# Kernel tuning notes

Hardware: AMD Instinct MI355X
Metric: run time of the kernel (lower is better)

The kernel has to match this reference:

```python
import jax, jax.numpy as jnp
import numpy as np

IN_DIM, LATENT = 512, 256
INTER, COMMAND, MOTOR = 18, 12, 3
STATE = INTER + COMMAND + MOTOR  # 33
B, T = 64, 512


def _make_mask(p, k, fanout=None, fanin=None, rng=None):
    # NCP-style sparse wiring: random fanout per source / fanin per destination.
    m = np.zeros((p, k), dtype=np.float32)
    if fanout is not None:
        for i in range(p):
            m[i, rng.choice(k, size=fanout, replace=False)] = 1.0
    if fanin is not None:
        for j in range(k):
            m[rng.choice(p, size=fanin, replace=False), j] = 1.0
    # WiredCfCCell appends dense (all-ones) recurrent block for the layer's own state
    full = np.concatenate([m, np.ones((k, k), np.float32)], axis=0)  # (p+k, k)
    return jnp.asarray(full.T)  # (k, p+k), matches nn.Linear weight layout


def setup_inputs() -> dict:
    key = jax.random.key(0)
    ks = iter(jax.random.split(key, 64))
    def nrm(shape, scale=0.1):
        return jax.random.normal(next(ks), shape, jnp.float32) * scale
    rng = np.random.default_rng(2222)
    inp = {}
    inp["x"] = jax.random.normal(next(ks), (B, T, IN_DIM), jnp.float32)
    inp["fc1_w"] = nrm((LATENT, IN_DIM), 0.02)
    inp["fc1_b"] = nrm((LATENT,))
    inp["lstm_wi"] = nrm((4 * STATE, LATENT), 0.05)
    inp["lstm_bi"] = nrm((4 * STATE,))
    inp["lstm_wh"] = nrm((4 * STATE, STATE))
    dims = [(LATENT, INTER), (INTER, COMMAND), (COMMAND, MOTOR)]
    for l, (p, k) in enumerate(dims):
        for nm in ("ff1w", "ff2w", "taw", "tbw"):
            inp[nm + str(l)] = nrm((k, p + k))
        for nm in ("ff1b", "ff2b", "tab", "tbb"):
            inp[nm + str(l)] = nrm((k,))
    fan = [dict(fanout=6), dict(fanout=4), dict(fanin=6)]
    for l, (p, k) in enumerate(dims):
        inp["mask" + str(l)] = _make_mask(p, k, rng=rng, **fan[l])
    return inp


def _forward(x, fc1_w, fc1_b, lstm_wi, lstm_bi, lstm_wh, layers, masks):
    # fc1 projection (dropout in module is never applied in forward)
    feats = jnp.einsum('btd,ld->btl', x, fc1_w) + fc1_b  # (B,T,LATENT)

    def step(carry, u):  # u: (B, LATENT)
        h, c = carry  # (B, STATE) each
        # mixed-memory LSTM cell (ncps LSTMCell: forget gate bias +1)
        z = u @ lstm_wi.T + lstm_bi + h @ lstm_wh.T
        ia, ig, fg, og = jnp.split(z, 4, axis=-1)
        c = c * jax.nn.sigmoid(fg + 1.0) + jnp.tanh(ia) * jax.nn.sigmoid(ig)
        h = jnp.tanh(c) * jax.nn.sigmoid(og)
        # WiredCfCCell: inter -> command -> motor, each a masked CfC cell (ts=1)
        hs = jnp.split(h, (INTER, INTER + COMMAND), axis=-1)
        inp_l = u
        new_hs = []
        for (w1, b1, w2, b2, aw, ab, bw, bb), m, hl in zip(layers, masks, hs):
            xc = jnp.concatenate([inp_l, hl], axis=-1)
            f1 = jnp.tanh(xc @ (w1 * m).T + b1)
            f2 = jnp.tanh(xc @ (w2 * m).T + b2)
            ti = jax.nn.sigmoid((xc @ aw.T + ab) + (xc @ bw.T + bb))  # t_a*ts + t_b, ts=1
            hl = f1 * (1.0 - ti) + ti * f2
            new_hs.append(hl)
            inp_l = hl
        return (jnp.concatenate(new_hs, axis=-1), c), new_hs[-1]

    h0 = jnp.zeros((x.shape[0], STATE), x.dtype)
    (_, _), ys = jax.lax.scan(step, (h0, h0), feats.transpose(1, 0, 2))
    return ys.transpose(1, 0, 2)  # (B, T, MOTOR)


def reference(x, fc1_w, fc1_b, lstm_wi, lstm_bi, lstm_wh,
              ff1w0, ff2w0, taw0, tbw0, ff1b0, ff2b0, tab0, tbb0,
              ff1w1, ff2w1, taw1, tbw1, ff1b1, ff2b1, tab1, tbb1,
              ff1w2, ff2w2, taw2, tbw2, ff1b2, ff2b2, tab2, tbb2,
              mask0, mask1, mask2):
    layers = [
        (ff1w0, ff1b0, ff2w0, ff2b0, taw0, tab0, tbw0, tbb0),
        (ff1w1, ff1b1, ff2w1, ff2b1, taw1, tab1, tbw1, tbb1),
        (ff1w2, ff1b2, ff2w2, ff2b2, taw2, tab2, tbw2, tbb2),
    ]
    return _forward(x, fc1_w, fc1_b, lstm_wi, lstm_bi, lstm_wh, layers, (mask0, mask1, mask2))
```

## Files before the change

kernel.cpp:

```cpp
#include <hip/hip_runtime.h>
#include <hip/hip_bf16.h>

#define BT 32768
#define TSTEPS 512
#define NBATCH 64
#define KDIM 512
#define NPAD 192
#define NW 192

#define L2E 1.4426950408889634f
#define T2E 2.8853900817779268f

__device__ __forceinline__ float rl(float v, int lane) {
    return __int_as_float(__builtin_amdgcn_readlane(__float_as_int(v), lane));
}
__device__ __forceinline__ float bperm(int byteidx, float v) {
    return __int_as_float(__builtin_amdgcn_ds_bpermute(byteidx, __float_as_int(v)));
}
__device__ __forceinline__ float actf(float x, float s, float sc, float a, float b) {
    float e = exp2f(fmaf(s, x, sc));
    return fmaf(a, __builtin_amdgcn_rcpf(1.f + e), b);
}

__global__ __launch_bounds__(256) void fold_kernel(
    const float* __restrict__ fc1_w, const float* __restrict__ fc1_b,
    const float* __restrict__ lstm_wi, const float* __restrict__ lstm_bi,
    const float* __restrict__ ff1w0, const float* __restrict__ ff2w0,
    const float* __restrict__ taw0, const float* __restrict__ tbw0,
    const float* __restrict__ ff1b0, const float* __restrict__ ff2b0,
    const float* __restrict__ tab0, const float* __restrict__ tbb0,
    const float* __restrict__ mask0,
    float* __restrict__ Wc, float* __restrict__ bc)
{
    const int o = blockIdx.x;
    const int t = threadIdx.x;
    __shared__ float wrow[256];
    __shared__ float red[256];

    float wl = 0.f, b0 = 0.f;
    if (o < 132) { wl = lstm_wi[o * 256 + t]; b0 = lstm_bi[o]; }
    else if (o < 186) {
        const int e = o - 132, m = e / 18, i = e - m * 18;
        if (m == 0)      { wl = ff1w0[i * 274 + t] * mask0[i * 274 + t]; b0 = ff1b0[i]; }
        else if (m == 1) { wl = ff2w0[i * 274 + t] * mask0[i * 274 + t]; b0 = ff2b0[i]; }
        else             { wl = taw0[i * 274 + t] + tbw0[i * 274 + t];   b0 = tab0[i] + tbb0[i]; }
    }
    wrow[t] = wl;
    __syncthreads();

    float acc0 = 0.f, acc1 = 0.f;
    for (int l = 0; l < 256; l++) {
        float w = wrow[l];
        acc0 = fmaf(fc1_w[l * 512 + t], w, acc0);
        acc1 = fmaf(fc1_w[l * 512 + t + 256], w, acc1);
    }
    Wc[(size_t)t * NW + o] = acc0;
    Wc[(size_t)(t + 256) * NW + o] = acc1;

    red[t] = fc1_b[t] * wl;
    __syncthreads();
    for (int s = 128; s > 0; s >>= 1) {
        if (t < s) red[t] += red[t + s];
        __syncthreads();
    }
    if (t == 0) bc[o] = red[0] + b0;
}

__global__ __launch_bounds__(256) void gemm_kernel(
    const float* __restrict__ X, const float* __restrict__ Wc,
    const float* __restrict__ bc, float* __restrict__ P)
{
    __shared__ float As[16][68];
    __shared__ float Bs[16][64];
    const int tid = threadIdx.x;
    const int m0 = blockIdx.x * 64;
    const int n0 = blockIdx.y * 64;
    const int lr = tid >> 2;
    const int lc = (tid & 3) << 2;
    const int wr = tid >> 4;
    const int wc = (tid & 15) << 2;
    const int tm = (tid >> 4) << 2;
    const int tn = (tid & 15) << 2;

    float acc[4][4];
#pragma unroll
    for (int i = 0; i < 4; i++)
#pragma unroll
        for (int j = 0; j < 4; j++) acc[i][j] = 0.f;

    for (int k0 = 0; k0 < KDIM; k0 += 16) {
        float4 av = *(const float4*)(X + (size_t)(m0 + lr) * KDIM + k0 + lc);
        float4 bv = *(const float4*)(Wc + (size_t)(k0 + wr) * NW + n0 + wc);
        __syncthreads();
        As[lc + 0][lr] = av.x; As[lc + 1][lr] = av.y;
        As[lc + 2][lr] = av.z; As[lc + 3][lr] = av.w;
        *(float4*)&Bs[wr][wc] = bv;
        __syncthreads();
#pragma unroll
        for (int k = 0; k < 16; k++) {
            float4 a = *(const float4*)&As[k][tm];
            float4 b = *(const float4*)&Bs[k][tn];
            acc[0][0] = fmaf(a.x, b.x, acc[0][0]); acc[0][1] = fmaf(a.x, b.y, acc[0][1]);
            acc[0][2] = fmaf(a.x, b.z, acc[0][2]); acc[0][3] = fmaf(a.x, b.w, acc[0][3]);
            acc[1][0] = fmaf(a.y, b.x, acc[1][0]); acc[1][1] = fmaf(a.y, b.y, acc[1][1]);
            acc[1][2] = fmaf(a.y, b.z, acc[1][2]); acc[1][3] = fmaf(a.y, b.w, acc[1][3]);
            acc[2][0] = fmaf(a.z, b.x, acc[2][0]); acc[2][1] = fmaf(a.z, b.y, acc[2][1]);
            acc[2][2] = fmaf(a.z, b.z, acc[2][2]); acc[2][3] = fmaf(a.z, b.w, acc[2][3]);
            acc[3][0] = fmaf(a.w, b.x, acc[3][0]); acc[3][1] = fmaf(a.w, b.y, acc[3][1]);
            acc[3][2] = fmaf(a.w, b.z, acc[3][2]); acc[3][3] = fmaf(a.w, b.w, acc[3][3]);
        }
    }

    {
        float4 bias = *(const float4*)(bc + n0 + tn);
#pragma unroll
        for (int i = 0; i < 4; i++) {
            float4 r;
            r.x = acc[i][0] + bias.x; r.y = acc[i][1] + bias.y;
            r.z = acc[i][2] + bias.z; r.w = acc[i][3] + bias.w;
            *(float4*)(P + (size_t)(m0 + tm + i) * NPAD + n0 + tn) = r;
        }
    }
}

__global__ __launch_bounds__(64)
__attribute__((amdgpu_waves_per_eu(1, 1)))
void scan_kernel(
    const float* __restrict__ P, const float* __restrict__ lstm_wh,
    const float* __restrict__ ff1w0, const float* __restrict__ ff2w0,
    const float* __restrict__ taw0, const float* __restrict__ tbw0,
    const float* __restrict__ ff1w1, const float* __restrict__ ff2w1,
    const float* __restrict__ taw1, const float* __restrict__ tbw1,
    const float* __restrict__ ff1b1, const float* __restrict__ ff2b1,
    const float* __restrict__ tab1, const float* __restrict__ tbb1,
    const float* __restrict__ ff1w2, const float* __restrict__ ff2w2,
    const float* __restrict__ taw2, const float* __restrict__ tbw2,
    const float* __restrict__ ff1b2, const float* __restrict__ ff2b2,
    const float* __restrict__ tab2, const float* __restrict__ tbb2,
    const float* __restrict__ mask1, const float* __restrict__ mask2,
    float* __restrict__ out)
{
    const int L = threadIdx.x;
    const int b = blockIdx.x;

    __shared__ float wCt[33 * 4];
    if (L < 33) {
        for (int j = 0; j < 4; j++) wCt[L * 4 + j] = lstm_wh[(128 + j) * 33 + L];
    }
    __syncthreads();
    const int jC = L & 3;

    float wA[33], wB[33];
#pragma unroll
    for (int k = 0; k < 33; k++) {
        wA[k] = lstm_wh[L * 33 + k];
        wB[k] = lstm_wh[(64 + L) * 33 + k];
    }
    float w0[18];
    {
        int e = L - 4; e = (e < 0) ? 0 : ((e > 53) ? 53 : e);
        const int m = e / 18, i = e - m * 18;
        const float* pa = (m == 0) ? ff1w0 : (m == 1) ? ff2w0 : taw0;
#pragma unroll
        for (int k = 0; k < 18; k++) {
            float w = pa[i * 274 + 256 + k];
            if (m == 2) w += tbw0[i * 274 + 256 + k];
            w0[k] = w;
        }
    }
    float w1[30], bias1;
    {
        const int d = (L < 36) ? L : 35;
        const int m = d / 12, i = d - m * 12;
        const float* pa = (m == 0) ? ff1w1 : (m == 1) ? ff2w1 : taw1;
#pragma unroll
        for (int k = 0; k < 30; k++) {
            float w = pa[i * 30 + k];
            if (m == 2) w += tbw1[i * 30 + k];
            else w *= mask1[i * 30 + k];
            w1[k] = w;
        }
        bias1 = (m == 0) ? ff1b1[i] : (m == 1) ? ff2b1[i] : (tab1[i] + tbb1[i]);
    }
    float w2[15], bias2;
    {
        const int d = (L < 9) ? L : 8;
        const int m = d / 3, i = d - m * 3;
        const float* pa = (m == 0) ? ff1w2 : (m == 1) ? ff2w2 : taw2;
#pragma unroll
        for (int k = 0; k < 15; k++) {
            float w = pa[i * 15 + k];
            if (m == 2) w += tbw2[i * 15 + k];
            else w *= mask2[i * 15 + k];
            w2[k] = w;
        }
        bias2 = (m == 0) ? ff1b2[i] : (m == 1) ? ff2b2[i] : (tab2[i] + tbb2[i]);
    }

    const float sA  = (L < 33) ? -T2E : -L2E;
    const float aA  = (L < 33) ? 2.f : 1.f;
    const float bA  = (L < 33) ? -1.f : 0.f;
    const float scB = (L >= 2 && L <= 34) ? -L2E : 0.f;
    const float s0  = (L < 40) ? -T2E : -L2E;
    const float a0c = (L < 40) ? 2.f : 1.f;
    const float b0c = (L < 40) ? -1.f : 0.f;
    const float s1  = (L < 24) ? -T2E : -L2E;
    const float a1c = (L < 24) ? 2.f : 1.f;
    const float b1c = (L < 24) ? -1.f : 0.f;
    const float s2  = (L < 6) ? -T2E : -L2E;
    const float a2c = (L < 6) ? 2.f : 1.f;
    const float b2c = (L < 6) ? -1.f : 0.f;

    const int xIgA = (4 * (33 + L)) & 255;
    const int xIgB = (4 * (L - 31)) & 255;
    const int xFg  = (4 * (2 + L)) & 255;
    const int xOgA = (4 * (35 + L)) & 255;
    const int xOgC = (4 * (L - 29)) & 255;
    const int x0f1 = (4 * (4 + L)) & 255;
    const int x0f2 = (4 * (22 + L)) & 255;
    const int x0ti = (4 * (40 + L)) & 255;
    const int x1f1 = (4 * L) & 255;
    const int x1f2 = (4 * (12 + L)) & 255;
    const int x1ti = (4 * (24 + L)) & 255;
    const int x2f1 = (4 * L) & 255;
    const int x2f2 = (4 * (3 + L)) & 255;
    const int x2ti = (4 * (6 + L)) & 255;

    float h[33];
#pragma unroll
    for (int k = 0; k < 33; k++) h[k] = 0.f;
    float cc = 0.f;

    const float* Pb = P + (size_t)b * TSTEPS * NPAD;
    float c1 = Pb[L], c2 = Pb[64 + L], c3 = Pb[128 + L];
    const float* P1 = Pb + NPAD;
    float n1 = P1[L], n2 = P1[64 + L], n3 = P1[128 + L];
    float* outp = out + (size_t)b * TSTEPS * 3 + L;

#pragma unroll 1
    for (int t = 0; t < TSTEPS; t++) {
        const int tf = (t + 2 < TSTEPS) ? t + 2 : TSTEPS - 1;
        const float* Pf = Pb + (size_t)tf * NPAD;
        const float f1p = Pf[L], f2p = Pf[64 + L], f3p = Pf[128 + L];

        float aA0 = c1, aA1 = 0.f, aB0 = c2, aB1 = 0.f, aC0 = c3, aC1 = 0.f;
#pragma unroll
        for (int k = 0; k < 32; k += 2) {
            aA0 = fmaf(wA[k],     h[k],     aA0);
            aA1 = fmaf(wA[k + 1], h[k + 1], aA1);
            aB0 = fmaf(wB[k],     h[k],     aB0);
            aB1 = fmaf(wB[k + 1], h[k + 1], aB1);
            aC0 = fmaf(wCt[k * 4 + jC],       h[k],     aC0);
            aC1 = fmaf(wCt[(k + 1) * 4 + jC], h[k + 1], aC1);
        }
        aA0 = fmaf(wA[32], h[32], aA0);
        aB0 = fmaf(wB[32], h[32], aB0);
        aC0 = fmaf(wCt[32 * 4 + jC], h[32], aC0);
        const float actA = actf(aA0 + aA1, sA, 0.f, aA, bA);
        const float actB = actf(aB0 + aB1, -L2E, scB, 1.f, 0.f);
        const float actC = actf(aC0 + aC1, -L2E, 0.f, 1.f, 0.f);
        const float gIgA = bperm(xIgA, actA);
        const float gIgB = bperm(xIgB, actB);
        const float gFg  = bperm(xFg, actB);
        const float gOgA = bperm(xOgA, actB);
        const float gOgC = bperm(xOgC, actC);
        const float IG = (L < 31) ? gIgA : gIgB;
        const float OG = (L < 29) ? gOgA : gOgC;
        cc = fmaf(cc, gFg, actA * IG);
        const float hv = actf(cc, -T2E, 0.f, 2.f, -1.f) * OG;

#pragma unroll
        for (int k = 0; k < 33; k++) h[k] = rl(hv, k);

        float l00 = c3, l01 = 0.f;
#pragma unroll
        for (int k = 0; k < 18; k += 2) {
            l00 = fmaf(w0[k],     h[k],     l00);
            l01 = fmaf(w0[k + 1], h[k + 1], l01);
        }
        {
            const float av = actf(l00 + l01, s0, 0.f, a0c, b0c);
            const float f1 = bperm(x0f1, av);
            const float f2 = bperm(x0f2, av);
            const float ti = bperm(x0ti, av);
            const float h0 = fmaf(ti, f2 - f1, f1);
#pragma unroll
            for (int k = 0; k < 18; k++) h[k] = rl(h0, k);
        }

        float l10 = bias1, l11 = 0.f;
#pragma unroll
        for (int k = 0; k < 30; k += 2) {
            l10 = fmaf(w1[k],     h[k],     l10);
            l11 = fmaf(w1[k + 1], h[k + 1], l11);
        }
        {
            const float av = actf(l10 + l11, s1, 0.f, a1c, b1c);
            const float f1 = bperm(x1f1, av);
            const float f2 = bperm(x1f2, av);
            const float ti = bperm(x1ti, av);
            const float h1 = fmaf(ti, f2 - f1, f1);
#pragma unroll
            for (int k = 0; k < 12; k++) h[18 + k] = rl(h1, k);
        }

        float l20 = bias2, l21 = 0.f;
#pragma unroll
        for (int k = 0; k < 14; k += 2) {
            l20 = fmaf(w2[k],     h[18 + k],     l20);
            l21 = fmaf(w2[k + 1], h[18 + k + 1], l21);
        }
        l20 = fmaf(w2[14], h[32], l20);
        {
            const float av = actf(l20 + l21, s2, 0.f, a2c, b2c);
            const float f1 = bperm(x2f1, av);
            const float f2 = bperm(x2f2, av);
            const float ti = bperm(x2ti, av);
            const float h2 = fmaf(ti, f2 - f1, f1);
            if (L < 3) outp[(size_t)t * 3] = h2;
            h[30] = rl(h2, 0); h[31] = rl(h2, 1); h[32] = rl(h2, 2);
        }

        c1 = n1; c2 = n2; c3 = n3;
        n1 = f1p; n2 = f2p; n3 = f3p;
    }
}

extern "C" void kernel_launch(void* const* d_in, const int* in_sizes, int n_in,
                              void* d_out, int out_size, void* d_ws, size_t ws_size,
                              hipStream_t stream) {
    const float* x       = (const float*)d_in[0];
    const float* fc1_w   = (const float*)d_in[1];
    const float* fc1_b   = (const float*)d_in[2];
    const float* lstm_wi = (const float*)d_in[3];
    const float* lstm_bi = (const float*)d_in[4];
    const float* lstm_wh = (const float*)d_in[5];
    const float* ff1w0 = (const float*)d_in[6];
    const float* ff2w0 = (const float*)d_in[7];
    const float* taw0  = (const float*)d_in[8];
    const float* tbw0  = (const float*)d_in[9];
    const float* ff1b0 = (const float*)d_in[10];
    const float* ff2b0 = (const float*)d_in[11];
    const float* tab0  = (const float*)d_in[12];
    const float* tbb0  = (const float*)d_in[13];
    const float* ff1w1 = (const float*)d_in[14];
    const float* ff2w1 = (const float*)d_in[15];
    const float* taw1  = (const float*)d_in[16];
    const float* tbw1  = (const float*)d_in[17];
    const float* ff1b1 = (const float*)d_in[18];
    const float* ff2b1 = (const float*)d_in[19];
    const float* tab1  = (const float*)d_in[20];
    const float* tbb1  = (const float*)d_in[21];
    const float* ff1w2 = (const float*)d_in[22];
    const float* ff2w2 = (const float*)d_in[23];
    const float* taw2  = (const float*)d_in[24];
    const float* tbw2  = (const float*)d_in[25];
    const float* ff1b2 = (const float*)d_in[26];
    const float* ff2b2 = (const float*)d_in[27];
    const float* tab2  = (const float*)d_in[28];
    const float* tbb2  = (const float*)d_in[29];
    const float* mask0 = (const float*)d_in[30];
    const float* mask1 = (const float*)d_in[31];
    const float* mask2 = (const float*)d_in[32];

    float* Wc = (float*)d_ws;
    float* bc = Wc + 512 * NW;
    float* P  = bc + NW;
    float* outp = (float*)d_out;

    fold_kernel<<<192, 256, 0, stream>>>(fc1_w, fc1_b, lstm_wi, lstm_bi,
                                         ff1w0, ff2w0, taw0, tbw0,
                                         ff1b0, ff2b0, tab0, tbb0, mask0, Wc, bc);
    gemm_kernel<<<dim3(BT / 64, 3), 256, 0, stream>>>(x, Wc, bc, P);
    scan_kernel<<<NBATCH, 64, 0, stream>>>(P, lstm_wh,
                                           ff1w0, ff2w0, taw0, tbw0,
                                           ff1w1, ff2w1, taw1, tbw1,
                                           ff1b1, ff2b1, tab1, tbb1,
                                           ff1w2, ff2w2, taw2, tbw2,
                                           ff1b2, ff2b2, tab2, tbb2,
                                           mask1, mask2, outp);
}
```

Before: 685.3 us.

## Interleave next-step LSTM gate accumulation into layer chain and split dot-product accumulators

Moves the LSTM recurrent gate dot products for the next timestep so they are accumulated piecewise as each layer's state becomes available, overlapping them with the serial layer-0/1/2 chain. The next step no longer starts with a 33-term dependent FMA chain before the activations. The partial sums for layers 1 and 2 that depend on the previous step's state are hoisted early, and the remaining dot products use four independent accumulators to shorten dependency latency. The trade-offs are higher register pressure and more complex scheduling, and the changed summation order can alter floating-point rounding slightly.

```diff
diff --git a/kernel.cpp b/kernel.cpp
--- a/kernel.cpp
+++ b/kernel.cpp
@@ -232,9 +232,10 @@
     float cc = 0.f;
 
     const float* Pb = P + (size_t)b * TSTEPS * NPAD;
-    float c1 = Pb[L], c2 = Pb[64 + L], c3 = Pb[128 + L];
+    float c3 = Pb[128 + L];
     const float* P1 = Pb + NPAD;
     float n1 = P1[L], n2 = P1[64 + L], n3 = P1[128 + L];
+    float gA = Pb[L], gB = Pb[64 + L], gC = c3;
     float* outp = out + (size_t)b * TSTEPS * 3 + L;
 
 #pragma unroll 1
@@ -243,22 +244,9 @@
         const float* Pf = Pb + (size_t)tf * NPAD;
         const float f1p = Pf[L], f2p = Pf[64 + L], f3p = Pf[128 + L];
 
-        float aA0 = c1, aA1 = 0.f, aB0 = c2, aB1 = 0.f, aC0 = c3, aC1 = 0.f;
-#pragma unroll
-        for (int k = 0; k < 32; k += 2) {
-            aA0 = fmaf(wA[k],     h[k],     aA0);
-            aA1 = fmaf(wA[k + 1], h[k + 1], aA1);
-            aB0 = fmaf(wB[k],     h[k],     aB0);
-            aB1 = fmaf(wB[k + 1], h[k + 1], aB1);
-            aC0 = fmaf(wCt[k * 4 + jC],       h[k],     aC0);
-            aC1 = fmaf(wCt[(k + 1) * 4 + jC], h[k + 1], aC1);
-        }
-        aA0 = fmaf(wA[32], h[32], aA0);
-        aB0 = fmaf(wB[32], h[32], aB0);
-        aC0 = fmaf(wCt[32 * 4 + jC], h[32], aC0);
-        const float actA = actf(aA0 + aA1, sA, 0.f, aA, bA);
-        const float actB = actf(aB0 + aB1, -L2E, scB, 1.f, 0.f);
-        const float actC = actf(aC0 + aC1, -L2E, 0.f, 1.f, 0.f);
+        const float actA = actf(gA, sA, 0.f, aA, bA);
+        const float actB = actf(gB, -L2E, scB, 1.f, 0.f);
+        const float actC = actf(gC, -L2E, 0.f, 1.f, 0.f);
         const float gIgA = bperm(xIgA, actA);
         const float gIgB = bperm(xIgB, actB);
         const float gFg  = bperm(xFg, actB);
@@ -270,16 +258,32 @@
         const float hv = actf(cc, -T2E, 0.f, 2.f, -1.f) * OG;
 
 #pragma unroll
-        for (int k = 0; k < 33; k++) h[k] = rl(hv, k);
-
-        float l00 = c3, l01 = 0.f;
-#pragma unroll
-        for (int k = 0; k < 18; k += 2) {
-            l00 = fmaf(w0[k],     h[k],     l00);
-            l01 = fmaf(w0[k + 1], h[k + 1], l01);
-        }
+        for (int k = 0; k < 18; k++) h[k] = rl(hv, k);
+
+        float A0 = c3, A1 = 0.f, A2 = 0.f, A3 = 0.f;
+#pragma unroll
+        for (int k = 0; k < 16; k += 4) {
+            A0 = fmaf(w0[k],     h[k],     A0);
+            A1 = fmaf(w0[k + 1], h[k + 1], A1);
+            A2 = fmaf(w0[k + 2], h[k + 2], A2);
+            A3 = fmaf(w0[k + 3], h[k + 3], A3);
+        }
+        A0 = fmaf(w0[16], h[16], A0);
+        A1 = fmaf(w0[17], h[17], A1);
+        const float l0 = (A0 + A1) + (A2 + A3);
+
+#pragma unroll
+        for (int k = 18; k < 33; k++) h[k] = rl(hv, k);
+        float l1p = bias1;
+#pragma unroll
+        for (int k = 18; k < 30; k++) l1p = fmaf(w1[k], h[k], l1p);
+        float l2p = bias2;
+        l2p = fmaf(w2[12], h[30], l2p);
+        l2p = fmaf(w2[13], h[31], l2p);
+        l2p = fmaf(w2[14], h[32], l2p);
+
         {
-            const float av = actf(l00 + l01, s0, 0.f, a0c, b0c);
+            const float av = actf(l0, s0, 0.f, a0c, b0c);
             const float f1 = bperm(x0f1, av);
             const float f2 = bperm(x0f2, av);
             const float ti = bperm(x0ti, av);
@@ -288,14 +292,27 @@
             for (int k = 0; k < 18; k++) h[k] = rl(h0, k);
         }
 
-        float l10 = bias1, l11 = 0.f;
-#pragma unroll
-        for (int k = 0; k < 30; k += 2) {
-            l10 = fmaf(w1[k],     h[k],     l10);
-            l11 = fmaf(w1[k + 1], h[k + 1], l11);
-        }
+        gA = n1; gB = n2; gC = n3;
+#pragma unroll
+        for (int k = 0; k < 18; k++) {
+            gA = fmaf(wA[k], h[k], gA);
+            gB = fmaf(wB[k], h[k], gB);
+            gC = fmaf(wCt[k * 4 + jC], h[k], gC);
+        }
+
+        float B0 = l1p, B1 = 0.f, B2 = 0.f, B3 = 0.f;
+#pragma unroll
+        for (int k = 0; k < 16; k += 4) {
+            B0 = fmaf(w1[k],     h[k],     B0);
+            B1 = fmaf(w1[k + 1], h[k + 1], B1);
+            B2 = fmaf(w1[k + 2], h[k + 2], B2);
+            B3 = fmaf(w1[k + 3], h[k + 3], B3);
+        }
+        B0 = fmaf(w1[16], h[16], B0);
+        B1 = fmaf(w1[17], h[17], B1);
+        const float l1 = (B0 + B1) + (B2 + B3);
         {
-            const float av = actf(l10 + l11, s1, 0.f, a1c, b1c);
+            const float av = actf(l1, s1, 0.f, a1c, b1c);
             const float f1 = bperm(x1f1, av);
             const float f2 = bperm(x1f2, av);
             const float ti = bperm(x1ti, av);
@@ -304,15 +321,24 @@
             for (int k = 0; k < 12; k++) h[18 + k] = rl(h1, k);
         }
 
-        float l20 = bias2, l21 = 0.f;
-#pragma unroll
-        for (int k = 0; k < 14; k += 2) {
-            l20 = fmaf(w2[k],     h[18 + k],     l20);
-            l21 = fmaf(w2[k + 1], h[18 + k + 1], l21);
-        }
-        l20 = fmaf(w2[14], h[32], l20);
+#pragma unroll
+        for (int k = 18; k < 30; k++) {
+            gA = fmaf(wA[k], h[k], gA);
+            gB = fmaf(wB[k], h[k], gB);
+            gC = fmaf(wCt[k * 4 + jC], h[k], gC);
+        }
+
+        float C0 = l2p, C1 = 0.f, C2 = 0.f, C3 = 0.f;
+#pragma unroll
+        for (int k = 0; k < 12; k += 4) {
+            C0 = fmaf(w2[k],     h[18 + k],     C0);
+            C1 = fmaf(w2[k + 1], h[18 + k + 1], C1);
+            C2 = fmaf(w2[k + 2], h[18 + k + 2], C2);
+            C3 = fmaf(w2[k + 3], h[18 + k + 3], C3);
+        }
+        const float l2 = (C0 + C1) + (C2 + C3);
         {
-            const float av = actf(l20 + l21, s2, 0.f, a2c, b2c);
+            const float av = actf(l2, s2, 0.f, a2c, b2c);
             const float f1 = bperm(x2f1, av);
             const float f2 = bperm(x2f2, av);
             const float ti = bperm(x2ti, av);
@@ -321,7 +347,14 @@
             h[30] = rl(h2, 0); h[31] = rl(h2, 1); h[32] = rl(h2, 2);
         }
 
-        c1 = n1; c2 = n2; c3 = n3;
+#pragma unroll
+        for (int k = 30; k < 33; k++) {
+            gA = fmaf(wA[k], h[k], gA);
+            gB = fmaf(wB[k], h[k], gB);
+            gC = fmaf(wCt[k * 4 + jC], h[k], gC);
+        }
+
+        c3 = n3;
         n1 = f1p; n2 = f2p; n3 = f3p;
     }
 }
```

New measurement: 621.5 us. -9.3%, faster.
